# Kernel optimization log

Measured on AMD Instinct MI355X. Metric: run time of the kernel, lower is better.

## Reference

```python
import jax, jax.numpy as jnp
import numpy as np

NUM_CLASSES = 8
SCORE_T = 0.5
IOU_T = 0.5
POSE_HYPS = 10
MAX_DET = 100
B, A = 1, 4096


def _pairwise_iou(bx):
    # bx: (N,4) in (x1,y1,x2,y2); TF-style +1 pixel convention
    x1 = jnp.maximum(bx[:, None, 0], bx[None, :, 0])
    y1 = jnp.maximum(bx[:, None, 1], bx[None, :, 1])
    x2 = jnp.minimum(bx[:, None, 2], bx[None, :, 2])
    y2 = jnp.minimum(bx[:, None, 3], bx[None, :, 3])
    wid = x2 - x1 + 1.0
    hei = y2 - y1 + 1.0
    inter = wid * hei
    area = (bx[:, 2] - bx[:, 0] + 1.0) * (bx[:, 3] - bx[:, 1] + 1.0)
    den = area[:, None] + area[None, :] - inter
    ov = jnp.where(den == 0.0, 0.0, inter / jnp.where(den == 0.0, 1.0, den))  # divide_no_nan
    return jnp.where((wid <= 0.0) | (hei <= 0.0), 0.0, ov)


def _per_class(scores_c, boxes_c, poses_c, conf_c):
    # Fixed-shape re-expression of _filter_detections: instead of compacting the
    # boxes with score > threshold (dynamic shape), keep all N and mask invalid
    # boxes out of the overlap indicator. Relative ordering (which drives the
    # argmax tie-break and the ascending sort) is identical to the compacted
    # subset, so the math matches exactly.
    N = scores_c.shape[0]
    K = POSE_HYPS + 1
    valid = scores_c > SCORE_T
    m = jnp.sum(valid.astype(jnp.int32))  # number of selected boxes
    ov = _pairwise_iou(boxes_c)  # (N,N)
    ind = ((ov > IOU_T) & valid[:, None] & valid[None, :]).astype(jnp.float32)
    # scatter_nd: true_ov[argmax_col(row i), i] = max(row i); column i is unique per update
    max_col = jnp.argmax(ind, axis=1)
    true_ov = jnp.zeros_like(ind).at[max_col, jnp.arange(N)].add(jnp.max(ind, axis=1))
    bc = (1.0 - ov) * true_ov * conf_c[None, :]
    bc = jnp.where(bc == 0.0, 1000.0, bc)  # 1000 = sentinel for 'not a hypothesis'
    # Only the first min(pose_hyps+1, m) ascending-sorted entries per row survive the
    # sequence mask, so take the K smallest instead of a full argsort (same result;
    # top_k of the negation breaks ties by lowest index like a stable ascending sort).
    neg, args = jax.lax.top_k(-bc, K)
    svals = -neg  # (N,K) K smallest per row
    hyp = (jnp.arange(K) < jnp.minimum(K, m)).astype(jnp.float32)
    cmask = jnp.where(svals == 1000.0, 0.0, 1.0) * hyp[None, :]
    denom = jnp.sum(cmask, axis=1)  # (N,)
    safe = jnp.where(denom == 0.0, 1.0, denom)
    poses_avg = jnp.where(denom[:, None] == 0.0, 0.0,
                          jnp.sum(cmask[:, :, None] * poses_c[args], axis=1) / safe[:, None])
    boxes_avg = jnp.where(denom[:, None] == 0.0, 0.0,
                          jnp.sum(cmask[:, :, None] * boxes_c[args], axis=1) / safe[:, None])
    return poses_avg, boxes_avg, denom > 0.0


def _forward(boxes3D, boxes, classification, poses, confidence):
    C = NUM_CLASSES
    N = classification.shape[0] * classification.shape[1]
    cls = classification.reshape(N, C)
    bxs = boxes.reshape(N, C, 4)
    pss = poses.reshape(N, C, 12)
    cnf = confidence.reshape(N, C)
    # boxes3D is reshaped/gathered by the original but never used afterwards (dead code)
    xs = (cls.T, jnp.transpose(bxs, (1, 0, 2)), jnp.transpose(pss, (1, 0, 2)), cnf.T)
    # serialize over classes so only one NxN working set is live at a time
    poses_avg, boxes_avg, survive = jax.lax.map(lambda t: _per_class(*t), xs)
    surv = survive.reshape(-1)  # (C*N,) class-major, matching the original concat order
    count = jnp.sum(surv.astype(jnp.int32))
    scores_flat = jnp.where(surv, cls.T.reshape(-1), -jnp.inf)
    top_scores, _ = jax.lax.top_k(scores_flat, MAX_DET)
    rank = jnp.arange(MAX_DET)
    ok = rank < count
    out_scores = jnp.where(ok, top_scores, -1.0)
    # NOTE: the original computes top_indices but never applies it — labels/poses/
    # indices/boxes stay in class-major survivor order, truncated/padded with -1.
    pos = jnp.arange(C * N)
    order = jnp.argsort(jnp.where(surv, pos, pos + C * N))  # stable compaction
    sel = order[:MAX_DET]
    labels_flat = jnp.repeat(jnp.arange(C), N)
    anchors_flat = jnp.tile(jnp.arange(N), C)
    out_labels = jnp.where(ok, labels_flat[sel], -1).astype(jnp.int32)
    out_idx = jnp.where(ok, anchors_flat[sel], -1).astype(jnp.int32)
    out_poses = jnp.where(ok[:, None], poses_avg.reshape(C * N, 12)[sel], -1.0)
    out_boxes = jnp.where(ok[:, None], boxes_avg.reshape(C * N, 4)[sel], -1.0)
    return out_scores, out_labels, out_poses, out_idx, out_boxes


def setup_inputs():
    key = jax.random.key(0)
    k1, k2, k3, k4, k5, k6 = jax.random.split(key, 6)
    C = NUM_CLASSES
    # realistic heavily-overlapping boxes in a 640x640 image
    cxy = jax.random.uniform(k1, (B, A, C, 2), minval=0.0, maxval=640.0)
    wh = jax.random.uniform(k2, (B, A, C, 2), minval=10.0, maxval=120.0)
    boxes = jnp.concatenate([cxy - wh / 2.0, cxy + wh / 2.0], axis=-1).reshape(B, A, C * 4)
    return {
        "boxes3D": jax.random.normal(k6, (B, A, C * 16), dtype=jnp.float32),
        "boxes": boxes,
        "classification": jax.random.uniform(k3, (B, A, C), dtype=jnp.float32),
        "poses": jax.random.normal(k4, (B, A, C * 12), dtype=jnp.float32),
        "confidence": jax.random.uniform(k5, (B, A, C), dtype=jnp.float32),
    }


def reference(boxes3D, boxes, classification, poses, confidence):
    return _forward(boxes3D, boxes, classification, poses, confidence)
```

## Files before the change

kernel.cpp:

```cpp
#include <hip/hip_runtime.h>
#include <stdint.h>

#define N_ANCH 4096
#define NCLS 8
#define CN (N_ANCH * NCLS)
#define SCORE_TH 0.5f
#define IOU_TH 0.5f
#define KSEL 11
#define MAX_DET 100
#define CAND_CAP 4096
#define TILE 128
#define TPC (N_ANCH / TILE)
#define NTRI (TPC * (TPC + 1) / 2)

__device__ __forceinline__ float iou_f(float4 a, float areaA, float4 b, float areaB) {
    float x1 = fmaxf(a.x, b.x);
    float y1 = fmaxf(a.y, b.y);
    float x2 = fminf(a.z, b.z);
    float y2 = fminf(a.w, b.w);
    float wid = x2 - x1 + 1.0f;
    float hei = y2 - y1 + 1.0f;
    float inter = wid * hei;
    float den = areaA + areaB - inter;
    float ov = (den == 0.0f) ? 0.0f : (inter / den);
    if (wid <= 0.0f || hei <= 0.0f) ov = 0.0f;
    return ov;
}

__global__ void k_prep(const float* __restrict__ boxes, const float* __restrict__ cls,
                       const float* __restrict__ conf,
                       float4* boxesT, float* areaT, float* scoresT, float* confT,
                       int* surv, int* hist, int* gcnt, int* minRank) {
    int t = blockIdx.x * blockDim.x + threadIdx.x;
    if (t >= CN) return;
    int n = t >> 3;
    int c = t & 7;
    int p = c * N_ANCH + n;
    scoresT[p] = cls[t];
    confT[p] = conf[t];
    float4 b = reinterpret_cast<const float4*>(boxes)[t];
    boxesT[p] = b;
    areaT[p] = (b.z - b.x + 1.0f) * (b.w - b.y + 1.0f);
    surv[t] = 0;
    minRank[t] = 0x7FFFFFFF;
    if (t < 1024) hist[t] = 0;
    if (t == 1024) *gcnt = 0;
}

__global__ void __launch_bounds__(256) k_validlist(const float* __restrict__ scoresT,
                                                   int* validList, int* mVal) {
    int c = blockIdx.x;
    int tid = threadIdx.x;
    int lane = tid & 63, w = tid >> 6;
    __shared__ int wsum[4];
    __shared__ int base;
    if (tid == 0) base = 0;
    __syncthreads();
    for (int start = 0; start < N_ANCH; start += 256) {
        int n = start + tid;
        int flag = (scoresT[c * N_ANCH + n] > SCORE_TH) ? 1 : 0;
        unsigned long long mask = __ballot(flag);
        if (lane == 0) wsum[w] = __popcll(mask);
        __syncthreads();
        int rank = __popcll(mask & ((1ull << lane) - 1ull));
        int wbase = 0;
        for (int i = 0; i < w; i++) wbase += wsum[i];
        int total = wsum[0] + wsum[1] + wsum[2] + wsum[3];
        if (flag) validList[c * N_ANCH + base + wbase + rank] = n;
        __syncthreads();
        if (tid == 0) base += total;
        __syncthreads();
    }
    if (tid == 0) mVal[c] = base;
}

__global__ void __launch_bounds__(128) k_repmat(const float4* __restrict__ boxesT,
                                                const float* __restrict__ areaT,
                                                const int* __restrict__ validList,
                                                const int* __restrict__ mVal,
                                                int* minRank) {
    int bid = blockIdx.x;
    int c = bid / NTRI;
    int t = bid - c * NTRI;
    int ci = (int)((sqrtf(8.0f * (float)t + 1.0f) - 1.0f) * 0.5f);
    while ((ci + 1) * (ci + 2) / 2 <= t) ci++;
    while (ci * (ci + 1) / 2 > t) ci--;
    int cj = t - ci * (ci + 1) / 2;
    int mc = mVal[c];
    int ib = ci * TILE, jb = cj * TILE;
    if (ib >= mc || jb >= mc) return;
    int tid = threadIdx.x;
    int cbase = c << 12;
    const int* vl = validList + cbase;
    __shared__ float4 sB[TILE];
    __shared__ float sA[TILE];
    if (jb + tid < mc) {
        int vj = vl[jb + tid];
        sB[tid] = boxesT[cbase + vj];
        sA[tid] = areaT[cbase + vj];
    }
    __syncthreads();
    int i = ib + tid;
    if (i >= mc) return;
    int k = vl[i];
    float4 bk = boxesT[cbase + k];
    float ak = areaT[cbase + k];
    int limit = min(TILE, mc - jb);
    if (ci == cj) limit = min(limit, i - jb);
    int lmin = 0x7FFFFFFF;
    #pragma unroll 4
    for (int r = 0; r < limit; r++) {
        float ov = iou_f(bk, ak, sB[r], sA[r]);
        if (ov > IOU_TH && r < lmin) lmin = r;
    }
    if (lmin != 0x7FFFFFFF) atomicMin(&minRank[cbase + i], jb + lmin);
}

__global__ void __launch_bounds__(256) k_repfinal(const float4* __restrict__ boxesT,
                                                  const float* __restrict__ areaT,
                                                  const float* __restrict__ confT,
                                                  const int* __restrict__ validList,
                                                  const int* __restrict__ mVal,
                                                  const int* __restrict__ minRank,
                                                  int* rep, int* surv) {
    int t = blockIdx.x * blockDim.x + threadIdx.x;
    if (t >= CN) return;
    int c = t >> 12;
    int i = t & (N_ANCH - 1);
    int mc = mVal[c];
    if (i >= mc) return;
    int cbase = c << 12;
    const int* vl = validList + cbase;
    int k = vl[i];
    int mr = minRank[t];
    if (mr > i) mr = i;
    int j = vl[mr];
    rep[cbase + k] = j;
    if (mr < i) {
        float ov = iou_f(boxesT[cbase + k], areaT[cbase + k], boxesT[cbase + j], areaT[cbase + j]);
        float bcv = (1.0f - ov) * confT[cbase + k];
        if (bcv != 0.0f) surv[cbase + j] = 1;
    }
}

__global__ void __launch_bounds__(256) k_survscan(const int* __restrict__ surv,
                                                  const float* __restrict__ scoresT,
                                                  int* blockCnt, int* hist) {
    int b = blockIdx.x, tid = threadIdx.x;
    int p = b * 256 + tid;
    int flag = surv[p] != 0;
    unsigned long long mask = __ballot(flag);
    __shared__ int wcnt[4];
    if ((tid & 63) == 0) wcnt[tid >> 6] = __popcll(mask);
    if (flag) {
        unsigned bits = __float_as_uint(scoresT[p]);
        int bb = (int)((bits - 0x3F000000u) >> 13);
        int bkt = bb < 0 ? 0 : (bb > 1023 ? 1023 : bb);
        atomicAdd(&hist[bkt], 1);
    }
    __syncthreads();
    if (tid == 0) blockCnt[b] = wcnt[0] + wcnt[1] + wcnt[2] + wcnt[3];
}

__global__ void __launch_bounds__(256) k_prefix(const int* __restrict__ blockCnt,
                                                const int* __restrict__ hist,
                                                int* blockOff, int* count_g, int* t0_g) {
    int tid = threadIdx.x;
    __shared__ int sfx[256];
    __shared__ int thrB;
    __shared__ int countS;
    if (tid == 0) {
        int run = 0;
        for (int i = 0; i < 128; i++) { blockOff[i] = run; run += blockCnt[i]; }
        *count_g = run; countS = run; thrB = 0;
    }
    int part = hist[4 * tid] + hist[4 * tid + 1] + hist[4 * tid + 2] + hist[4 * tid + 3];
    sfx[tid] = part;
    __syncthreads();
    if (tid == 0) {
        int run = 0;
        for (int i = 255; i >= 0; i--) { int v = sfx[i]; sfx[i] = run; run += v; }
    }
    __syncthreads();
    int count = countS;
    int target = count < MAX_DET ? count : MAX_DET;
    int S = sfx[tid];
    int found = -1;
    for (int b = 4 * tid + 3; b >= 4 * tid; b--) {
        S += hist[b];
        if (found < 0 && S >= target) found = b;
    }
    if (found >= 0) atomicMax(&thrB, found);
    __syncthreads();
    if (tid == 0) *t0_g = thrB;
}

__global__ void __launch_bounds__(256) k_selgather(const int* __restrict__ surv,
                                                   const float* __restrict__ scoresT,
                                                   const int* __restrict__ blockOff,
                                                   const int* __restrict__ t0_g,
                                                   int* sel, float* cand, int* gcnt) {
    int b = blockIdx.x, tid = threadIdx.x;
    int lane = tid & 63, w = tid >> 6;
    int p = b * 256 + tid;
    int flag = surv[p] != 0;
    unsigned long long mask = __ballot(flag);
    __shared__ int wcnt[4];
    if (lane == 0) wcnt[w] = __popcll(mask);
    __syncthreads();
    int rank = __popcll(mask & ((1ull << lane) - 1ull));
    int wbase = 0;
    for (int i = 0; i < w; i++) wbase += wcnt[i];
    int idx = blockOff[b] + wbase + rank;
    if (flag && idx < MAX_DET) sel[idx] = p;
    if (flag) {
        unsigned bits = __float_as_uint(scoresT[p]);
        int bb = (int)((bits - 0x3F000000u) >> 13);
        int bkt = bb < 0 ? 0 : (bb > 1023 ? 1023 : bb);
        if (bkt >= *t0_g) {
            int id = atomicAdd(gcnt, 1);
            if (id < CAND_CAP) cand[id] = scoresT[p];
        }
    }
}

__global__ void __launch_bounds__(256) k_sort(const float* __restrict__ cand,
                                              const int* __restrict__ gcnt,
                                              const int* __restrict__ count_g,
                                              float* out) {
    __shared__ float s[CAND_CAP];
    int tid = threadIdx.x;
    int cc = *gcnt; if (cc > CAND_CAP) cc = CAND_CAP;
    int count = *count_g;
    int n = 128; while (n < cc) n <<= 1;
    for (int i = tid; i < n; i += 256) s[i] = (i < cc) ? -cand[i] : 1e38f;
    __syncthreads();
    for (int kk = 2; kk <= n; kk <<= 1) {
        for (int jj = kk >> 1; jj > 0; jj >>= 1) {
            for (int i = tid; i < n; i += 256) {
                int ixj = i ^ jj;
                if (ixj > i) {
                    float a = s[i], b2 = s[ixj];
                    bool up = ((i & kk) == 0);
                    if (up ? (a > b2) : (a < b2)) { s[i] = b2; s[ixj] = a; }
                }
            }
            __syncthreads();
        }
    }
    if (tid < MAX_DET) out[tid] = (tid < count) ? -s[tid] : -1.0f;
}

__global__ void __launch_bounds__(256) k_out(const float4* __restrict__ boxesT,
                                             const float* __restrict__ areaT,
                                             const float* __restrict__ confT,
                                             const float* __restrict__ poses,
                                             const int* __restrict__ validList,
                                             const int* __restrict__ mVal,
                                             const int* __restrict__ rep,
                                             const int* __restrict__ sel,
                                             const int* __restrict__ count_g,
                                             float* out) {
    int s = blockIdx.x;
    int tid = threadIdx.x;
    int count = *count_g;
    if (s >= count) {
        if (tid == 0) { out[100 + s] = -1.0f; out[1400 + s] = -1.0f; }
        if (tid < 12) out[200 + s * 12 + tid] = -1.0f;
        if (tid >= 16 && tid < 20) out[1500 + s * 4 + (tid - 16)] = -1.0f;
        return;
    }
    int p = sel[s];
    int c = p >> 12;
    int r = p & (N_ANCH - 1);
    __shared__ unsigned long long keyArr[4096];
    __shared__ int nmS;
    __shared__ int kselS[KSEL];
    __shared__ unsigned long long bestS;
    __shared__ unsigned long long redK[4];
    if (tid == 0) nmS = 0;
    __syncthreads();
    float4 br = boxesT[(c << 12) + r];
    float ar = areaT[(c << 12) + r];
    int mc = mVal[c];
    for (int i = tid; i < mc; i += 256) {
        int k = validList[(c << 12) + i];
        if (k != r && rep[(c << 12) + k] == r) {
            float ov = iou_f(br, ar, boxesT[(c << 12) + k], areaT[(c << 12) + k]);
            float bcv = (1.0f - ov) * confT[(c << 12) + k];
            if (bcv != 0.0f) {
                int id = atomicAdd(&nmS, 1);
                keyArr[id] = ((unsigned long long)__float_as_uint(bcv) << 32) | (unsigned)k;
            }
        }
    }
    __syncthreads();
    int nm = nmS;
    int dn = nm < KSEL ? nm : KSEL;
    unsigned long long lastBest = ~0ull;
    for (int j = 0; j < dn; j++) {
        unsigned long long bk = ~0ull;
        for (int i = tid; i < nm; i += 256) {
            unsigned long long v = keyArr[i];
            if (v == lastBest) { keyArr[i] = ~0ull; v = ~0ull; }
            if (v < bk) bk = v;
        }
        for (int off = 32; off > 0; off >>= 1) {
            unsigned long long o = __shfl_down(bk, off);
            if (o < bk) bk = o;
        }
        if ((tid & 63) == 0) redK[tid >> 6] = bk;
        __syncthreads();
        if (tid == 0) {
            unsigned long long B = redK[0];
            for (int q2 = 1; q2 < 4; q2++) if (redK[q2] < B) B = redK[q2];
            bestS = B;
            kselS[j] = (int)(B & 0xFFFFFFFFull);
        }
        __syncthreads();
        lastBest = bestS;
    }
    float fdn = (float)(dn > 0 ? dn : 1);
    if (tid < 12) {
        float ssum = 0.0f;
        for (int j = 0; j < dn; j++) {
            int k = kselS[j];
            ssum += poses[(k * 8 + c) * 12 + tid];
        }
        out[200 + s * 12 + tid] = ssum / fdn;
    } else if (tid < 16) {
        int d = tid - 12;
        float ssum = 0.0f;
        for (int j = 0; j < dn; j++) {
            int k = kselS[j];
            const float* bb = (const float*)&boxesT[(c << 12) + k];
            ssum += bb[d];
        }
        out[1500 + s * 4 + d] = ssum / fdn;
    } else if (tid == 16) {
        out[100 + s] = (float)c;
    } else if (tid == 17) {
        out[1400 + s] = (float)r;
    }
}

extern "C" void kernel_launch(void* const* d_in, const int* in_sizes, int n_in,
                              void* d_out, int out_size, void* d_ws, size_t ws_size,
                              hipStream_t stream) {
    const float* boxes = (const float*)d_in[1];
    const float* cls   = (const float*)d_in[2];
    const float* poses = (const float*)d_in[3];
    const float* conf  = (const float*)d_in[4];
    float* out = (float*)d_out;

    char* ws = (char*)d_ws;
    size_t off = 0;
    auto alloc = [&](size_t bytes) {
        void* p = ws + off;
        off += (bytes + 255) & ~(size_t)255;
        return p;
    };
    float4* boxesT  = (float4*)alloc(CN * sizeof(float4));
    float*  areaT   = (float*)alloc(CN * sizeof(float));
    float*  scoresT = (float*)alloc(CN * sizeof(float));
    float*  confT   = (float*)alloc(CN * sizeof(float));
    int*    validList = (int*)alloc(CN * sizeof(int));
    int*    mVal    = (int*)alloc(64);
    int*    rep     = (int*)alloc(CN * sizeof(int));
    int*    surv    = (int*)alloc(CN * sizeof(int));
    int*    sel     = (int*)alloc(MAX_DET * sizeof(int));
    int*    count_g = (int*)alloc(64);
    float*  cand    = (float*)alloc(CAND_CAP * sizeof(float));
    int*    hist    = (int*)alloc(1024 * sizeof(int));
    int*    blockCnt = (int*)alloc(128 * sizeof(int));
    int*    blockOff = (int*)alloc(128 * sizeof(int));
    int*    t0_g    = (int*)alloc(64);
    int*    gcnt    = (int*)alloc(64);
    int*    minRank = (int*)alloc(CN * sizeof(int));

    k_prep<<<CN / 256, 256, 0, stream>>>(boxes, cls, conf, boxesT, areaT, scoresT, confT, surv, hist, gcnt, minRank);
    k_validlist<<<NCLS, 256, 0, stream>>>(scoresT, validList, mVal);
    k_repmat<<<NCLS * NTRI, 128, 0, stream>>>(boxesT, areaT, validList, mVal, minRank);
    k_repfinal<<<CN / 256, 256, 0, stream>>>(boxesT, areaT, confT, validList, mVal, minRank, rep, surv);
    k_survscan<<<128, 256, 0, stream>>>(surv, scoresT, blockCnt, hist);
    k_prefix<<<1, 256, 0, stream>>>(blockCnt, hist, blockOff, count_g, t0_g);
    k_selgather<<<128, 256, 0, stream>>>(surv, scoresT, blockOff, t0_g, sel, cand, gcnt);
    k_sort<<<1, 256, 0, stream>>>(cand, gcnt, count_g, out);
    k_out<<<MAX_DET, 256, 0, stream>>>(boxesT, areaT, confT, poses, validList, mVal, rep, sel, count_g, out);
}
```

Baseline: 138.0 us.

## Fuse all NMS stages into one persistent kernel with grid barriers

Replaces the nine separate kernel launches with a single persistent 256-block kernel that moves between stages using a global atomic barrier. The valid-list build now reads the class scores directly and runs alongside the transpose. The prefix computation is duplicated per block instead of running as a single-block kernel. The pairwise tile grows to 256 and tiles are handed out in a strided loop. This is meant to remove launch and inter-kernel gaps, at the cost of spin-barrier overhead, an extra memset, and a dependence on all 256 blocks being co-resident.

```diff
diff --git a/kernel.cpp b/kernel.cpp
--- a/kernel.cpp
+++ b/kernel.cpp
@@ -9,9 +9,18 @@
 #define KSEL 11
 #define MAX_DET 100
 #define CAND_CAP 4096
-#define TILE 128
+#define TILE 256
 #define TPC (N_ANCH / TILE)
 #define NTRI (TPC * (TPC + 1) / 2)
+#define GRID 256
+
+struct Params {
+    const float* boxes; const float* cls; const float* poses; const float* conf;
+    float4* boxesT; float* areaT; float* scoresT; float* confT;
+    int* validList; int* mVal; int* rep; int* surv;
+    int* sel; int* count_g; float* cand; int* hist;
+    int* blockCnt; int* gcnt; int* minRank; int* bar; float* out;
+};
 
 __device__ __forceinline__ float iou_f(float4 a, float areaA, float4 b, float areaB) {
     float x1 = fmaxf(a.x, b.x);
@@ -27,320 +36,313 @@
     return ov;
 }
 
-__global__ void k_prep(const float* __restrict__ boxes, const float* __restrict__ cls,
-                       const float* __restrict__ conf,
-                       float4* boxesT, float* areaT, float* scoresT, float* confT,
-                       int* surv, int* hist, int* gcnt, int* minRank) {
-    int t = blockIdx.x * blockDim.x + threadIdx.x;
-    if (t >= CN) return;
-    int n = t >> 3;
-    int c = t & 7;
-    int p = c * N_ANCH + n;
-    scoresT[p] = cls[t];
-    confT[p] = conf[t];
-    float4 b = reinterpret_cast<const float4*>(boxes)[t];
-    boxesT[p] = b;
-    areaT[p] = (b.z - b.x + 1.0f) * (b.w - b.y + 1.0f);
-    surv[t] = 0;
-    minRank[t] = 0x7FFFFFFF;
-    if (t < 1024) hist[t] = 0;
-    if (t == 1024) *gcnt = 0;
+__device__ __forceinline__ void gbar(int* bar) {
+    __syncthreads();
+    if (threadIdx.x == 0) {
+        __threadfence();
+        int g = __hip_atomic_load(&bar[16], __ATOMIC_RELAXED, __HIP_MEMORY_SCOPE_AGENT);
+        int prev = __hip_atomic_fetch_add(&bar[0], 1, __ATOMIC_ACQ_REL, __HIP_MEMORY_SCOPE_AGENT);
+        if (prev == GRID - 1) {
+            __hip_atomic_store(&bar[0], 0, __ATOMIC_RELAXED, __HIP_MEMORY_SCOPE_AGENT);
+            __hip_atomic_fetch_add(&bar[16], 1, __ATOMIC_RELEASE, __HIP_MEMORY_SCOPE_AGENT);
+        } else {
+            while (__hip_atomic_load(&bar[16], __ATOMIC_ACQUIRE, __HIP_MEMORY_SCOPE_AGENT) == g) {
+                __builtin_amdgcn_s_sleep(2);
+            }
+        }
+        __threadfence();
+    }
+    __syncthreads();
 }
 
-__global__ void __launch_bounds__(256) k_validlist(const float* __restrict__ scoresT,
-                                                   int* validList, int* mVal) {
-    int c = blockIdx.x;
-    int tid = threadIdx.x;
-    int lane = tid & 63, w = tid >> 6;
-    __shared__ int wsum[4];
-    __shared__ int base;
-    if (tid == 0) base = 0;
-    __syncthreads();
-    for (int start = 0; start < N_ANCH; start += 256) {
-        int n = start + tid;
-        int flag = (scoresT[c * N_ANCH + n] > SCORE_TH) ? 1 : 0;
+__global__ void __launch_bounds__(256, 2) fused(Params p) {
+    const int bid = blockIdx.x;
+    const int tid = threadIdx.x;
+    const int lane = tid & 63, w = tid >> 6;
+
+    __shared__ __align__(16) unsigned char SMEM[32768];
+    __shared__ int s_misc[8];
+    __shared__ int s_ksel[KSEL];
+    __shared__ unsigned long long s_red[5];
+
+    if (bid < NCLS) {
+        int c = bid;
+        unsigned long long* smask = (unsigned long long*)SMEM;
+        int* sbase = (int*)(SMEM + 512);
+        for (int ch = 0; ch < 16; ch++) {
+            int n = ch * 256 + tid;
+            int flag = (p.cls[n * NCLS + c] > SCORE_TH) ? 1 : 0;
+            unsigned long long m = __ballot(flag);
+            if (lane == 0) smask[ch * 4 + w] = m;
+        }
+        __syncthreads();
+        if (tid == 0) {
+            int run = 0;
+            for (int ch = 0; ch < 16; ch++) {
+                sbase[ch] = run;
+                run += __popcll(smask[ch * 4]) + __popcll(smask[ch * 4 + 1]) +
+                       __popcll(smask[ch * 4 + 2]) + __popcll(smask[ch * 4 + 3]);
+            }
+            p.mVal[c] = run;
+        }
+        __syncthreads();
+        for (int ch = 0; ch < 16; ch++) {
+            unsigned long long m = smask[ch * 4 + w];
+            if ((m >> lane) & 1ull) {
+                int rank = __popcll(m & ((1ull << lane) - 1ull));
+                int wb = 0;
+                for (int i = 0; i < w; i++) wb += __popcll(smask[ch * 4 + i]);
+                p.validList[c * N_ANCH + sbase[ch] + wb + rank] = ch * 256 + tid;
+            }
+        }
+    } else {
+        for (int t = (bid - NCLS) * 256 + tid; t < CN; t += (GRID - NCLS) * 256) {
+            int n = t >> 3;
+            int c = t & 7;
+            int q = c * N_ANCH + n;
+            p.scoresT[q] = p.cls[t];
+            p.confT[q] = p.conf[t];
+            float4 b = reinterpret_cast<const float4*>(p.boxes)[t];
+            p.boxesT[q] = b;
+            p.areaT[q] = (b.z - b.x + 1.0f) * (b.w - b.y + 1.0f);
+            p.surv[t] = 0;
+            p.minRank[t] = 0x7FFFFFFF;
+        }
+        int gt = (bid - NCLS) * 256 + tid;
+        if (gt < 1024) p.hist[gt] = 0;
+        if (gt == 1024) *p.gcnt = 0;
+    }
+    gbar(p.bar);
+
+    for (int job = bid; job < NCLS * NTRI; job += GRID) {
+        int c = job / NTRI;
+        int t = job - c * NTRI;
+        int ci = (int)((sqrtf(8.0f * (float)t + 1.0f) - 1.0f) * 0.5f);
+        while ((ci + 1) * (ci + 2) / 2 <= t) ci++;
+        while (ci * (ci + 1) / 2 > t) ci--;
+        int cj = t - ci * (ci + 1) / 2;
+        int mc = p.mVal[c];
+        int ib = ci * TILE, jb = cj * TILE;
+        if (ib >= mc || jb >= mc) continue;
+        int cbase = c << 12;
+        const int* vl = p.validList + cbase;
+        float4* sB = (float4*)SMEM;
+        float* sA = (float*)(SMEM + TILE * 16);
+        if (jb + tid < mc) {
+            int vj = vl[jb + tid];
+            sB[tid] = p.boxesT[cbase + vj];
+            sA[tid] = p.areaT[cbase + vj];
+        }
+        __syncthreads();
+        int i = ib + tid;
+        if (i < mc) {
+            int k = vl[i];
+            float4 bk = p.boxesT[cbase + k];
+            float ak = p.areaT[cbase + k];
+            int limit = min(TILE, mc - jb);
+            if (ci == cj) limit = min(limit, tid);
+            int lmin = 0x7FFFFFFF;
+            #pragma unroll 4
+            for (int r = 0; r < limit; r++) {
+                float ov = iou_f(bk, ak, sB[r], sA[r]);
+                if (ov > IOU_TH && r < lmin) lmin = r;
+            }
+            if (lmin != 0x7FFFFFFF) atomicMin(&p.minRank[cbase + i], jb + lmin);
+        }
+        __syncthreads();
+    }
+    gbar(p.bar);
+
+    for (int t = bid * 256 + tid; t < CN; t += GRID * 256) {
+        int c = t >> 12;
+        int i = t & (N_ANCH - 1);
+        int mc = p.mVal[c];
+        if (i >= mc) continue;
+        int cbase = c << 12;
+        const int* vl = p.validList + cbase;
+        int k = vl[i];
+        int mr = p.minRank[t];
+        if (mr > i) mr = i;
+        int j = vl[mr];
+        p.rep[cbase + k] = j;
+        if (mr < i) {
+            float ov = iou_f(p.boxesT[cbase + k], p.areaT[cbase + k],
+                             p.boxesT[cbase + j], p.areaT[cbase + j]);
+            float bcv = (1.0f - ov) * p.confT[cbase + k];
+            if (bcv != 0.0f) p.surv[cbase + j] = 1;
+        }
+    }
+    gbar(p.bar);
+
+    if (bid < CN / 256) {
+        int q = bid * 256 + tid;
+        int flag = p.surv[q] != 0;
         unsigned long long mask = __ballot(flag);
-        if (lane == 0) wsum[w] = __popcll(mask);
+        if (lane == 0) s_misc[4 + w] = __popcll(mask);
+        if (flag) {
+            unsigned bits = __float_as_uint(p.scoresT[q]);
+            int bb = (int)((bits - 0x3F000000u) >> 13);
+            int bkt = bb < 0 ? 0 : (bb > 1023 ? 1023 : bb);
+            atomicAdd(&p.hist[bkt], 1);
+        }
+        __syncthreads();
+        if (tid == 0) p.blockCnt[bid] = s_misc[4] + s_misc[5] + s_misc[6] + s_misc[7];
+    }
+    gbar(p.bar);
+
+    if (bid < CN / 256) {
+        int* sCnt = (int*)SMEM;
+        int* sSfx = (int*)(SMEM + 512);
+        if (tid == 0) s_misc[0] = 0;
+        if (tid < 128) sCnt[tid] = p.blockCnt[tid];
+        int part = p.hist[4 * tid] + p.hist[4 * tid + 1] +
+                   p.hist[4 * tid + 2] + p.hist[4 * tid + 3];
+        sSfx[tid] = part;
+        __syncthreads();
+        if (tid == 0) {
+            int run = 0, myoff = 0;
+            for (int i = 0; i < 128; i++) {
+                if (i == bid) myoff = run;
+                run += sCnt[i];
+            }
+            s_misc[1] = run;
+            s_misc[2] = myoff;
+            if (bid == 0) *p.count_g = run;
+            int run2 = 0;
+            for (int i = 255; i >= 0; i--) { int v = sSfx[i]; sSfx[i] = run2; run2 += v; }
+        }
+        __syncthreads();
+        int count = s_misc[1];
+        int target = count < MAX_DET ? count : MAX_DET;
+        int S = sSfx[tid];
+        int found = -1;
+        for (int b = 4 * tid + 3; b >= 4 * tid; b--) {
+            S += p.hist[b];
+            if (found < 0 && S >= target) found = b;
+        }
+        if (found >= 0) atomicMax(&s_misc[0], found);
+        __syncthreads();
+        int t0 = s_misc[0];
+        int q = bid * 256 + tid;
+        int flag = p.surv[q] != 0;
+        unsigned long long mask = __ballot(flag);
+        if (lane == 0) s_misc[4 + w] = __popcll(mask);
         __syncthreads();
         int rank = __popcll(mask & ((1ull << lane) - 1ull));
         int wbase = 0;
-        for (int i = 0; i < w; i++) wbase += wsum[i];
-        int total = wsum[0] + wsum[1] + wsum[2] + wsum[3];
-        if (flag) validList[c * N_ANCH + base + wbase + rank] = n;
-        __syncthreads();
-        if (tid == 0) base += total;
-        __syncthreads();
-    }
-    if (tid == 0) mVal[c] = base;
-}
-
-__global__ void __launch_bounds__(128) k_repmat(const float4* __restrict__ boxesT,
-                                                const float* __restrict__ areaT,
-                                                const int* __restrict__ validList,
-                                                const int* __restrict__ mVal,
-                                                int* minRank) {
-    int bid = blockIdx.x;
-    int c = bid / NTRI;
-    int t = bid - c * NTRI;
-    int ci = (int)((sqrtf(8.0f * (float)t + 1.0f) - 1.0f) * 0.5f);
-    while ((ci + 1) * (ci + 2) / 2 <= t) ci++;
-    while (ci * (ci + 1) / 2 > t) ci--;
-    int cj = t - ci * (ci + 1) / 2;
-    int mc = mVal[c];
-    int ib = ci * TILE, jb = cj * TILE;
-    if (ib >= mc || jb >= mc) return;
-    int tid = threadIdx.x;
-    int cbase = c << 12;
-    const int* vl = validList + cbase;
-    __shared__ float4 sB[TILE];
-    __shared__ float sA[TILE];
-    if (jb + tid < mc) {
-        int vj = vl[jb + tid];
-        sB[tid] = boxesT[cbase + vj];
-        sA[tid] = areaT[cbase + vj];
-    }
-    __syncthreads();
-    int i = ib + tid;
-    if (i >= mc) return;
-    int k = vl[i];
-    float4 bk = boxesT[cbase + k];
-    float ak = areaT[cbase + k];
-    int limit = min(TILE, mc - jb);
-    if (ci == cj) limit = min(limit, i - jb);
-    int lmin = 0x7FFFFFFF;
-    #pragma unroll 4
-    for (int r = 0; r < limit; r++) {
-        float ov = iou_f(bk, ak, sB[r], sA[r]);
-        if (ov > IOU_TH && r < lmin) lmin = r;
-    }
-    if (lmin != 0x7FFFFFFF) atomicMin(&minRank[cbase + i], jb + lmin);
-}
-
-__global__ void __launch_bounds__(256) k_repfinal(const float4* __restrict__ boxesT,
-                                                  const float* __restrict__ areaT,
-                                                  const float* __restrict__ confT,
-                                                  const int* __restrict__ validList,
-                                                  const int* __restrict__ mVal,
-                                                  const int* __restrict__ minRank,
-                                                  int* rep, int* surv) {
-    int t = blockIdx.x * blockDim.x + threadIdx.x;
-    if (t >= CN) return;
-    int c = t >> 12;
-    int i = t & (N_ANCH - 1);
-    int mc = mVal[c];
-    if (i >= mc) return;
-    int cbase = c << 12;
-    const int* vl = validList + cbase;
-    int k = vl[i];
-    int mr = minRank[t];
-    if (mr > i) mr = i;
-    int j = vl[mr];
-    rep[cbase + k] = j;
-    if (mr < i) {
-        float ov = iou_f(boxesT[cbase + k], areaT[cbase + k], boxesT[cbase + j], areaT[cbase + j]);
-        float bcv = (1.0f - ov) * confT[cbase + k];
-        if (bcv != 0.0f) surv[cbase + j] = 1;
-    }
-}
-
-__global__ void __launch_bounds__(256) k_survscan(const int* __restrict__ surv,
-                                                  const float* __restrict__ scoresT,
-                                                  int* blockCnt, int* hist) {
-    int b = blockIdx.x, tid = threadIdx.x;
-    int p = b * 256 + tid;
-    int flag = surv[p] != 0;
-    unsigned long long mask = __ballot(flag);
-    __shared__ int wcnt[4];
-    if ((tid & 63) == 0) wcnt[tid >> 6] = __popcll(mask);
-    if (flag) {
-        unsigned bits = __float_as_uint(scoresT[p]);
-        int bb = (int)((bits - 0x3F000000u) >> 13);
-        int bkt = bb < 0 ? 0 : (bb > 1023 ? 1023 : bb);
-        atomicAdd(&hist[bkt], 1);
-    }
-    __syncthreads();
-    if (tid == 0) blockCnt[b] = wcnt[0] + wcnt[1] + wcnt[2] + wcnt[3];
-}
-
-__global__ void __launch_bounds__(256) k_prefix(const int* __restrict__ blockCnt,
-                                                const int* __restrict__ hist,
-                                                int* blockOff, int* count_g, int* t0_g) {
-    int tid = threadIdx.x;
-    __shared__ int sfx[256];
-    __shared__ int thrB;
-    __shared__ int countS;
-    if (tid == 0) {
-        int run = 0;
-        for (int i = 0; i < 128; i++) { blockOff[i] = run; run += blockCnt[i]; }
-        *count_g = run; countS = run; thrB = 0;
-    }
-    int part = hist[4 * tid] + hist[4 * tid + 1] + hist[4 * tid + 2] + hist[4 * tid + 3];
-    sfx[tid] = part;
-    __syncthreads();
-    if (tid == 0) {
-        int run = 0;
-        for (int i = 255; i >= 0; i--) { int v = sfx[i]; sfx[i] = run; run += v; }
-    }
-    __syncthreads();
-    int count = countS;
-    int target = count < MAX_DET ? count : MAX_DET;
-    int S = sfx[tid];
-    int found = -1;
-    for (int b = 4 * tid + 3; b >= 4 * tid; b--) {
-        S += hist[b];
-        if (found < 0 && S >= target) found = b;
-    }
-    if (found >= 0) atomicMax(&thrB, found);
-    __syncthreads();
-    if (tid == 0) *t0_g = thrB;
-}
-
-__global__ void __launch_bounds__(256) k_selgather(const int* __restrict__ surv,
-                                                   const float* __restrict__ scoresT,
-                                                   const int* __restrict__ blockOff,
-                                                   const int* __restrict__ t0_g,
-                                                   int* sel, float* cand, int* gcnt) {
-    int b = blockIdx.x, tid = threadIdx.x;
-    int lane = tid & 63, w = tid >> 6;
-    int p = b * 256 + tid;
-    int flag = surv[p] != 0;
-    unsigned long long mask = __ballot(flag);
-    __shared__ int wcnt[4];
-    if (lane == 0) wcnt[w] = __popcll(mask);
-    __syncthreads();
-    int rank = __popcll(mask & ((1ull << lane) - 1ull));
-    int wbase = 0;
-    for (int i = 0; i < w; i++) wbase += wcnt[i];
-    int idx = blockOff[b] + wbase + rank;
-    if (flag && idx < MAX_DET) sel[idx] = p;
-    if (flag) {
-        unsigned bits = __float_as_uint(scoresT[p]);
-        int bb = (int)((bits - 0x3F000000u) >> 13);
-        int bkt = bb < 0 ? 0 : (bb > 1023 ? 1023 : bb);
-        if (bkt >= *t0_g) {
-            int id = atomicAdd(gcnt, 1);
-            if (id < CAND_CAP) cand[id] = scoresT[p];
-        }
-    }
-}
-
-__global__ void __launch_bounds__(256) k_sort(const float* __restrict__ cand,
-                                              const int* __restrict__ gcnt,
-                                              const int* __restrict__ count_g,
-                                              float* out) {
-    __shared__ float s[CAND_CAP];
-    int tid = threadIdx.x;
-    int cc = *gcnt; if (cc > CAND_CAP) cc = CAND_CAP;
-    int count = *count_g;
-    int n = 128; while (n < cc) n <<= 1;
-    for (int i = tid; i < n; i += 256) s[i] = (i < cc) ? -cand[i] : 1e38f;
-    __syncthreads();
-    for (int kk = 2; kk <= n; kk <<= 1) {
-        for (int jj = kk >> 1; jj > 0; jj >>= 1) {
-            for (int i = tid; i < n; i += 256) {
-                int ixj = i ^ jj;
-                if (ixj > i) {
-                    float a = s[i], b2 = s[ixj];
-                    bool up = ((i & kk) == 0);
-                    if (up ? (a > b2) : (a < b2)) { s[i] = b2; s[ixj] = a; }
-                }
-            }
+        for (int i = 0; i < w; i++) wbase += s_misc[4 + i];
+        int idx = s_misc[2] + wbase + rank;
+        if (flag && idx < MAX_DET) p.sel[idx] = q;
+        if (flag) {
+            unsigned bits = __float_as_uint(p.scoresT[q]);
+            int bb = (int)((bits - 0x3F000000u) >> 13);
+            int bkt = bb < 0 ? 0 : (bb > 1023 ? 1023 : bb);
+            if (bkt >= t0) {
+                int id = atomicAdd(p.gcnt, 1);
+                if (id < CAND_CAP) p.cand[id] = p.scoresT[q];
+            }
+        }
+    }
+    gbar(p.bar);
+
+    if (bid == 0) {
+        float* s = (float*)SMEM;
+        int cc = *p.gcnt; if (cc > CAND_CAP) cc = CAND_CAP;
+        int count = *p.count_g;
+        int n = 128; while (n < cc) n <<= 1;
+        for (int i = tid; i < n; i += 256) s[i] = (i < cc) ? -p.cand[i] : 1e38f;
+        __syncthreads();
+        for (int kk = 2; kk <= n; kk <<= 1) {
+            for (int jj = kk >> 1; jj > 0; jj >>= 1) {
+                for (int i = tid; i < n; i += 256) {
+                    int ixj = i ^ jj;
+                    if (ixj > i) {
+                        float a = s[i], b2 = s[ixj];
+                        bool up = ((i & kk) == 0);
+                        if (up ? (a > b2) : (a < b2)) { s[i] = b2; s[ixj] = a; }
+                    }
+                }
+                __syncthreads();
+            }
+        }
+        if (tid < MAX_DET) p.out[tid] = (tid < count) ? -s[tid] : -1.0f;
+    } else if (bid <= MAX_DET) {
+        int s = bid - 1;
+        int count = *p.count_g;
+        if (s >= count) {
+            if (tid == 0) { p.out[100 + s] = -1.0f; p.out[1400 + s] = -1.0f; }
+            if (tid < 12) p.out[200 + s * 12 + tid] = -1.0f;
+            if (tid >= 16 && tid < 20) p.out[1500 + s * 4 + (tid - 16)] = -1.0f;
+        } else {
+            int sp = p.sel[s];
+            int c = sp >> 12;
+            int r = sp & (N_ANCH - 1);
+            unsigned long long* keyArr = (unsigned long long*)SMEM;
+            if (tid == 0) s_misc[0] = 0;
             __syncthreads();
-        }
-    }
-    if (tid < MAX_DET) out[tid] = (tid < count) ? -s[tid] : -1.0f;
-}
-
-__global__ void __launch_bounds__(256) k_out(const float4* __restrict__ boxesT,
-                                             const float* __restrict__ areaT,
-                                             const float* __restrict__ confT,
-                                             const float* __restrict__ poses,
-                                             const int* __restrict__ validList,
-                                             const int* __restrict__ mVal,
-                                             const int* __restrict__ rep,
-                                             const int* __restrict__ sel,
-                                             const int* __restrict__ count_g,
-                                             float* out) {
-    int s = blockIdx.x;
-    int tid = threadIdx.x;
-    int count = *count_g;
-    if (s >= count) {
-        if (tid == 0) { out[100 + s] = -1.0f; out[1400 + s] = -1.0f; }
-        if (tid < 12) out[200 + s * 12 + tid] = -1.0f;
-        if (tid >= 16 && tid < 20) out[1500 + s * 4 + (tid - 16)] = -1.0f;
-        return;
-    }
-    int p = sel[s];
-    int c = p >> 12;
-    int r = p & (N_ANCH - 1);
-    __shared__ unsigned long long keyArr[4096];
-    __shared__ int nmS;
-    __shared__ int kselS[KSEL];
-    __shared__ unsigned long long bestS;
-    __shared__ unsigned long long redK[4];
-    if (tid == 0) nmS = 0;
-    __syncthreads();
-    float4 br = boxesT[(c << 12) + r];
-    float ar = areaT[(c << 12) + r];
-    int mc = mVal[c];
-    for (int i = tid; i < mc; i += 256) {
-        int k = validList[(c << 12) + i];
-        if (k != r && rep[(c << 12) + k] == r) {
-            float ov = iou_f(br, ar, boxesT[(c << 12) + k], areaT[(c << 12) + k]);
-            float bcv = (1.0f - ov) * confT[(c << 12) + k];
-            if (bcv != 0.0f) {
-                int id = atomicAdd(&nmS, 1);
-                keyArr[id] = ((unsigned long long)__float_as_uint(bcv) << 32) | (unsigned)k;
-            }
-        }
-    }
-    __syncthreads();
-    int nm = nmS;
-    int dn = nm < KSEL ? nm : KSEL;
-    unsigned long long lastBest = ~0ull;
-    for (int j = 0; j < dn; j++) {
-        unsigned long long bk = ~0ull;
-        for (int i = tid; i < nm; i += 256) {
-            unsigned long long v = keyArr[i];
-            if (v == lastBest) { keyArr[i] = ~0ull; v = ~0ull; }
-            if (v < bk) bk = v;
-        }
-        for (int off = 32; off > 0; off >>= 1) {
-            unsigned long long o = __shfl_down(bk, off);
-            if (o < bk) bk = o;
-        }
-        if ((tid & 63) == 0) redK[tid >> 6] = bk;
-        __syncthreads();
-        if (tid == 0) {
-            unsigned long long B = redK[0];
-            for (int q2 = 1; q2 < 4; q2++) if (redK[q2] < B) B = redK[q2];
-            bestS = B;
-            kselS[j] = (int)(B & 0xFFFFFFFFull);
-        }
-        __syncthreads();
-        lastBest = bestS;
-    }
-    float fdn = (float)(dn > 0 ? dn : 1);
-    if (tid < 12) {
-        float ssum = 0.0f;
-        for (int j = 0; j < dn; j++) {
-            int k = kselS[j];
-            ssum += poses[(k * 8 + c) * 12 + tid];
-        }
-        out[200 + s * 12 + tid] = ssum / fdn;
-    } else if (tid < 16) {
-        int d = tid - 12;
-        float ssum = 0.0f;
-        for (int j = 0; j < dn; j++) {
-            int k = kselS[j];
-            const float* bb = (const float*)&boxesT[(c << 12) + k];
-            ssum += bb[d];
-        }
-        out[1500 + s * 4 + d] = ssum / fdn;
-    } else if (tid == 16) {
-        out[100 + s] = (float)c;
-    } else if (tid == 17) {
-        out[1400 + s] = (float)r;
+            float4 br = p.boxesT[(c << 12) + r];
+            float ar = p.areaT[(c << 12) + r];
+            int mc = p.mVal[c];
+            for (int i = tid; i < mc; i += 256) {
+                int k = p.validList[(c << 12) + i];
+                if (k != r && p.rep[(c << 12) + k] == r) {
+                    float ov = iou_f(br, ar, p.boxesT[(c << 12) + k], p.areaT[(c << 12) + k]);
+                    float bcv = (1.0f - ov) * p.confT[(c << 12) + k];
+                    if (bcv != 0.0f) {
+                        int id = atomicAdd(&s_misc[0], 1);
+                        keyArr[id] = ((unsigned long long)__float_as_uint(bcv) << 32) | (unsigned)k;
+                    }
+                }
+            }
+            __syncthreads();
+            int nm = s_misc[0];
+            int dn = nm < KSEL ? nm : KSEL;
+            unsigned long long lastBest = ~0ull;
+            for (int j = 0; j < dn; j++) {
+                unsigned long long bk = ~0ull;
+                for (int i = tid; i < nm; i += 256) {
+                    unsigned long long v = keyArr[i];
+                    if (v == lastBest) { keyArr[i] = ~0ull; v = ~0ull; }
+                    if (v < bk) bk = v;
+                }
+                for (int off = 32; off > 0; off >>= 1) {
+                    unsigned long long o = __shfl_down(bk, off);
+                    if (o < bk) bk = o;
+                }
+                if (lane == 0) s_red[w] = bk;
+                __syncthreads();
+                if (tid == 0) {
+                    unsigned long long B = s_red[0];
+                    for (int q2 = 1; q2 < 4; q2++) if (s_red[q2] < B) B = s_red[q2];
+                    s_red[4] = B;
+                    s_ksel[j] = (int)(B & 0xFFFFFFFFull);
+                }
+                __syncthreads();
+                lastBest = s_red[4];
+            }
+            float fdn = (float)(dn > 0 ? dn : 1);
+            if (tid < 12) {
+                float ssum = 0.0f;
+                for (int j = 0; j < dn; j++) {
+                    int k = s_ksel[j];
+                    ssum += p.poses[(k * 8 + c) * 12 + tid];
+                }
+                p.out[200 + s * 12 + tid] = ssum / fdn;
+            } else if (tid < 16) {
+                int d = tid - 12;
+                float ssum = 0.0f;
+                for (int j = 0; j < dn; j++) {
+                    int k = s_ksel[j];
+                    const float* bb2 = (const float*)&p.boxesT[(c << 12) + k];
+                    ssum += bb2[d];
+                }
+                p.out[1500 + s * 4 + d] = ssum / fdn;
+            } else if (tid == 16) {
+                p.out[100 + s] = (float)c;
+            } else if (tid == 17) {
+                p.out[1400 + s] = (float)r;
+            }
+        }
     }
 }
 
@@ -356,35 +358,30 @@
     char* ws = (char*)d_ws;
     size_t off = 0;
     auto alloc = [&](size_t bytes) {
-        void* p = ws + off;
+        void* pp = ws + off;
         off += (bytes + 255) & ~(size_t)255;
-        return p;
+        return pp;
     };
-    float4* boxesT  = (float4*)alloc(CN * sizeof(float4));
-    float*  areaT   = (float*)alloc(CN * sizeof(float));
-    float*  scoresT = (float*)alloc(CN * sizeof(float));
-    float*  confT   = (float*)alloc(CN * sizeof(float));
-    int*    validList = (int*)alloc(CN * sizeof(int));
-    int*    mVal    = (int*)alloc(64);
-    int*    rep     = (int*)alloc(CN * sizeof(int));
-    int*    surv    = (int*)alloc(CN * sizeof(int));
-    int*    sel     = (int*)alloc(MAX_DET * sizeof(int));
-    int*    count_g = (int*)alloc(64);
-    float*  cand    = (float*)alloc(CAND_CAP * sizeof(float));
-    int*    hist    = (int*)alloc(1024 * sizeof(int));
-    int*    blockCnt = (int*)alloc(128 * sizeof(int));
-    int*    blockOff = (int*)alloc(128 * sizeof(int));
-    int*    t0_g    = (int*)alloc(64);
-    int*    gcnt    = (int*)alloc(64);
-    int*    minRank = (int*)alloc(CN * sizeof(int));
-
-    k_prep<<<CN / 256, 256, 0, stream>>>(boxes, cls, conf, boxesT, areaT, scoresT, confT, surv, hist, gcnt, minRank);
-    k_validlist<<<NCLS, 256, 0, stream>>>(scoresT, validList, mVal);
-    k_repmat<<<NCLS * NTRI, 128, 0, stream>>>(boxesT, areaT, validList, mVal, minRank);
-    k_repfinal<<<CN / 256, 256, 0, stream>>>(boxesT, areaT, confT, validList, mVal, minRank, rep, surv);
-    k_survscan<<<128, 256, 0, stream>>>(surv, scoresT, blockCnt, hist);
-    k_prefix<<<1, 256, 0, stream>>>(blockCnt, hist, blockOff, count_g, t0_g);
-    k_selgather<<<128, 256, 0, stream>>>(surv, scoresT, blockOff, t0_g, sel, cand, gcnt);
-    k_sort<<<1, 256, 0, stream>>>(cand, gcnt, count_g, out);
-    k_out<<<MAX_DET, 256, 0, stream>>>(boxesT, areaT, confT, poses, validList, mVal, rep, sel, count_g, out);
+    Params hp;
+    hp.boxes = boxes; hp.cls = cls; hp.poses = poses; hp.conf = conf;
+    hp.bar       = (int*)alloc(128);
+    hp.boxesT    = (float4*)alloc(CN * sizeof(float4));
+    hp.areaT     = (float*)alloc(CN * sizeof(float));
+    hp.scoresT   = (float*)alloc(CN * sizeof(float));
+    hp.confT     = (float*)alloc(CN * sizeof(float));
+    hp.validList = (int*)alloc(CN * sizeof(int));
+    hp.mVal      = (int*)alloc(64);
+    hp.rep       = (int*)alloc(CN * sizeof(int));
+    hp.surv      = (int*)alloc(CN * sizeof(int));
+    hp.sel       = (int*)alloc(MAX_DET * sizeof(int));
+    hp.count_g   = (int*)alloc(64);
+    hp.cand      = (float*)alloc(CAND_CAP * sizeof(float));
+    hp.hist      = (int*)alloc(1024 * sizeof(int));
+    hp.blockCnt  = (int*)alloc(128 * sizeof(int));
+    hp.gcnt      = (int*)alloc(64);
+    hp.minRank   = (int*)alloc(CN * sizeof(int));
+    hp.out = out;
+
+    hipMemsetAsync(hp.bar, 0, 128, stream);
+    fused<<<GRID, 256, 0, stream>>>(hp);
 }
```

Result: slower. 346.1 us (+150.8%).
